# Kernel tuning notes

Hardware: AMD Instinct MI355X
Metric: run time of the kernel (lower is better)

## Reference

```python
import jax, jax.numpy as jnp
import numpy as np

B, T, I = 256, 64, 512
H, C = 512, 97
MAXLEN = 25


def setup_inputs() -> dict:
    key = jax.random.key(0)
    ks = jax.random.split(key, 10)
    s_i = 1.0 / np.sqrt(I)
    s_h = 1.0 / np.sqrt(H)
    s_x = 1.0 / np.sqrt(I + C)
    return {
        "batch_hidden": jax.random.normal(ks[0], (B, T, I), jnp.float32),
        "context": jax.random.randint(ks[1], (B, MAXLEN + 1), 0, C),
        "max_length": MAXLEN,
        "train_mode": 1,
        "W_i2h": jax.random.normal(ks[2], (H, I), jnp.float32) * s_i,
        "W_h2h": jax.random.normal(ks[3], (H, H), jnp.float32) * s_h,
        "b_h2h": jnp.zeros((H,), jnp.float32),
        "w_score": jax.random.normal(ks[4], (1, H), jnp.float32) * s_h,
        "W_ih": jax.random.normal(ks[5], (4 * H, I + C), jnp.float32) * s_x,
        "b_ih": jnp.zeros((4 * H,), jnp.float32),
        "W_hh": jax.random.normal(ks[6], (4 * H, H), jnp.float32) * s_h,
        "b_hh": jnp.zeros((4 * H,), jnp.float32),
        "W_cls": jax.random.normal(ks[7], (C, H), jnp.float32) * s_h,
        "b_cls": jnp.zeros((C,), jnp.float32),
    }


def reference(batch_hidden, context, max_length, train_mode,
              W_i2h, W_h2h, b_h2h, w_score,
              W_ih, b_ih, W_hh, b_hh, W_cls, b_cls):
    steps = int(max_length) + 1
    b, t, _ = batch_hidden.shape
    h_dim = W_h2h.shape[0]
    n_cls = W_cls.shape[0]
    dt = batch_hidden.dtype

    # input_to_hidden(batch_hidden) is step-independent: hoist out of the loop.
    proj = jnp.einsum('bti,hi->bth', batch_hidden, W_i2h)  # [B,T,H]
    sv = w_score[0]  # [H]

    def cell(h, c, onehot):
        prev_proj = h @ W_h2h.T + b_h2h                       # [B,H]
        score = jnp.einsum('bth,h->bt', jnp.tanh(proj + prev_proj[:, None, :]), sv)
        attn = jax.nn.softmax(score, axis=1)                  # [B,T]
        ctx = jnp.einsum('bt,bti->bi', attn, batch_hidden)    # [B,I]
        x = jnp.concatenate([ctx, onehot], axis=1)            # [B,I+C]
        gates = x @ W_ih.T + b_ih + h @ W_hh.T + b_hh          # [B,4H]
        i_g, f_g, g_g, o_g = jnp.split(gates, 4, axis=1)
        c_new = jax.nn.sigmoid(f_g) * c + jax.nn.sigmoid(i_g) * jnp.tanh(g_g)
        h_new = jax.nn.sigmoid(o_g) * jnp.tanh(c_new)
        return h_new, c_new

    h0 = jnp.zeros((b, h_dim), dt)
    c0 = jnp.zeros((b, h_dim), dt)

    if train_mode:
        onehots = jax.nn.one_hot(context.T[:steps], n_cls, dtype=dt)  # [steps,B,C]

        def step(carry, oh):
            h, c = carry
            h, c = cell(h, c, oh)
            return (h, c), h

        _, hs = jax.lax.scan(step, (h0, c0), onehots)
        hidden_outputs = jnp.transpose(hs, (1, 0, 2))          # [B,steps,H]
        probs = hidden_outputs @ W_cls.T + b_cls               # [B,steps,C]
    else:
        def step(carry, _):
            h, c, tgt = carry
            oh = jax.nn.one_hot(tgt, n_cls, dtype=dt)
            h, c = cell(h, c, oh)
            p = h @ W_cls.T + b_cls
            return (h, c, jnp.argmax(p, axis=1)), p

        tgt0 = jnp.zeros((b,), jnp.int32)
        _, ps = jax.lax.scan(step, (h0, c0, tgt0), None, length=steps)
        probs = jnp.transpose(ps, (1, 0, 2))
    return probs
```

## Files before the change

kernel.cpp:

```cpp
#include <hip/hip_runtime.h>

#define BB 256
#define TT 64
#define HH 512
#define CC 97
#define SS 26
#define KX 1024

typedef __attribute__((ext_vector_type(8))) short short8;
typedef __attribute__((ext_vector_type(4))) float f32x4;

#define MFMA16(a, b, c) __builtin_amdgcn_mfma_f32_16x16x32_bf16((a), (b), (c), 0, 0, 0)

__device__ __forceinline__ unsigned short f2bf(float x) {
  unsigned int u = __float_as_uint(x);
  u += 0x7FFFu + ((u >> 16) & 1u);
  return (unsigned short)(u >> 16);
}
__device__ __forceinline__ float bf2f(unsigned short b) {
  return __uint_as_float(((unsigned int)b) << 16);
}
__device__ __forceinline__ void split8(float4 a, float4 b, short8& vh, short8& vl) {
  float x[8] = {a.x, a.y, a.z, a.w, b.x, b.y, b.z, b.w};
#pragma unroll
  for (int i = 0; i < 8; ++i) {
    unsigned short h = f2bf(x[i]);
    vh[i] = (short)h;
    vl[i] = (short)f2bf(x[i] - bf2f(h));
  }
}

__global__ __launch_bounds__(256) void k_init(float4* __restrict__ p, int n4) {
  int i = blockIdx.x * 256 + threadIdx.x;
  if (i < n4) p[i] = make_float4(0.f, 0.f, 0.f, 0.f);
}

__global__ __launch_bounds__(256) void k_prep_wp(const float* __restrict__ W_ih, const float* __restrict__ b_ih,
                                                 const float* __restrict__ W_hh, const float* __restrict__ b_hh,
                                                 unsigned short* __restrict__ Wp_hi, unsigned short* __restrict__ Wp_lo,
                                                 float* __restrict__ bp2, float* __restrict__ Woh2) {
  int p = blockIdx.x;
  int ntile = p >> 6, q = (p >> 4) & 3, jl = p & 15;
  int g = q * 512 + ntile * 16 + jl;
  int tid = threadIdx.x;
  for (int k = tid; k < 1024; k += 256) {
    float v = (k < 512) ? W_ih[(size_t)g * 609 + k] : W_hh[(size_t)g * 512 + (k - 512)];
    unsigned short h = f2bf(v);
    Wp_hi[(size_t)p * 1024 + k] = h;
    Wp_lo[(size_t)p * 1024 + k] = f2bf(v - bf2f(h));
  }
  if (tid < CC) Woh2[(size_t)p * CC + tid] = W_ih[(size_t)g * 609 + 512 + tid];
  if (tid == 0) bp2[p] = b_ih[g] + b_hh[g];
}

__global__ __launch_bounds__(256) void k_prep_w2h(const float* __restrict__ W_h2h,
                                                  unsigned short* __restrict__ Whi, unsigned short* __restrict__ Wlo) {
  int n = blockIdx.x;
  int tid = threadIdx.x;
  for (int k = tid; k < 512; k += 256) {
    float v = W_h2h[(size_t)n * 512 + k];
    unsigned short h = f2bf(v);
    Whi[(size_t)n * 512 + k] = h;
    Wlo[(size_t)n * 512 + k] = f2bf(v - bf2f(h));
  }
}

__global__ __launch_bounds__(256) void k0_proj(const float* __restrict__ A, const float* __restrict__ Bw,
                                               unsigned short* __restrict__ projb) {
  __shared__ short Ah[128][40], Al[128][40], Bh[64][40], Bl[64][40];
  int mt = blockIdx.x >> 3, nt = blockIdx.x & 7;
  int m0 = mt * 128, n0 = nt * 64;
  int tid = threadIdx.x;
  int w = tid >> 6, l = tid & 63;
  int wm = w >> 1, wn = w & 1;
  f32x4 acc[4][2];
#pragma unroll
  for (int i = 0; i < 4; ++i)
#pragma unroll
    for (int j = 0; j < 2; ++j) acc[i][j] = (f32x4){0.f, 0.f, 0.f, 0.f};
  int ar_s = tid >> 1, akc = (tid & 1) * 16;
  int br_s = tid >> 2, bkc = (tid & 3) * 8;
  for (int k0 = 0; k0 < 512; k0 += 32) {
    {
      const float* s = &A[(size_t)(m0 + ar_s) * 512 + k0 + akc];
      short8 vh, vl;
      split8(*(const float4*)s, *(const float4*)(s + 4), vh, vl);
      *(short8*)&Ah[ar_s][akc] = vh; *(short8*)&Al[ar_s][akc] = vl;
      split8(*(const float4*)(s + 8), *(const float4*)(s + 12), vh, vl);
      *(short8*)&Ah[ar_s][akc + 8] = vh; *(short8*)&Al[ar_s][akc + 8] = vl;
      const float* sb = &Bw[(size_t)(n0 + br_s) * 512 + k0 + bkc];
      split8(*(const float4*)sb, *(const float4*)(sb + 4), vh, vl);
      *(short8*)&Bh[br_s][bkc] = vh; *(short8*)&Bl[br_s][bkc] = vl;
    }
    __syncthreads();
    int ko = (l >> 4) * 8;
    short8 ah[4], al8[4];
#pragma unroll
    for (int mf = 0; mf < 4; ++mf) {
      int ar = wm * 64 + mf * 16 + (l & 15);
      ah[mf] = *(short8*)&Ah[ar][ko];
      al8[mf] = *(short8*)&Al[ar][ko];
    }
#pragma unroll
    for (int nf = 0; nf < 2; ++nf) {
      int br = wn * 32 + nf * 16 + (l & 15);
      short8 bh8 = *(short8*)&Bh[br][ko];
      short8 bl8 = *(short8*)&Bl[br][ko];
#pragma unroll
      for (int mf = 0; mf < 4; ++mf) {
        acc[mf][nf] = MFMA16(ah[mf], bh8, acc[mf][nf]);
        acc[mf][nf] = MFMA16(ah[mf], bl8, acc[mf][nf]);
        acc[mf][nf] = MFMA16(al8[mf], bh8, acc[mf][nf]);
      }
    }
    __syncthreads();
  }
#pragma unroll
  for (int mf = 0; mf < 4; ++mf)
#pragma unroll
    for (int nf = 0; nf < 2; ++nf)
#pragma unroll
      for (int r = 0; r < 4; ++r) {
        int m = m0 + wm * 64 + mf * 16 + (l >> 4) * 4 + r;
        int n = n0 + wn * 32 + nf * 16 + (l & 15);
        projb[(size_t)m * 512 + n] = f2bf(acc[mf][nf][r]);
      }
}

__global__ __launch_bounds__(256) void k1_pp(const float* __restrict__ xc, const unsigned short* __restrict__ Whi,
                                             const unsigned short* __restrict__ Wlo, float* __restrict__ pp) {
  __shared__ short Ah[64][40], Al[64][40], Bh[64][40], Bl[64][40];
  int bt = blockIdx.x & 3, nt = blockIdx.x >> 2;
  int b0 = bt * 64, n0 = nt * 64;
  int tid = threadIdx.x, w = tid >> 6, l = tid & 63;
  int wm = w >> 1, wn = w & 1;
  f32x4 acc[2][2];
#pragma unroll
  for (int i = 0; i < 2; ++i)
#pragma unroll
    for (int j = 0; j < 2; ++j) acc[i][j] = (f32x4){0.f, 0.f, 0.f, 0.f};
  int row = tid >> 2, kc = (tid & 3) * 8;
  for (int k0 = 0; k0 < 512; k0 += 32) {
    {
      const float* s = &xc[(size_t)(b0 + row) * KX + 512 + k0 + kc];
      short8 vh, vl;
      split8(*(const float4*)s, *(const float4*)(s + 4), vh, vl);
      *(short8*)&Ah[row][kc] = vh; *(short8*)&Al[row][kc] = vl;
      *(short8*)&Bh[row][kc] = *(const short8*)&Whi[(size_t)(n0 + row) * 512 + k0 + kc];
      *(short8*)&Bl[row][kc] = *(const short8*)&Wlo[(size_t)(n0 + row) * 512 + k0 + kc];
    }
    __syncthreads();
    int ko = (l >> 4) * 8;
    short8 ah[2], al8[2];
#pragma unroll
    for (int mf = 0; mf < 2; ++mf) {
      int ar = wm * 32 + mf * 16 + (l & 15);
      ah[mf] = *(short8*)&Ah[ar][ko];
      al8[mf] = *(short8*)&Al[ar][ko];
    }
#pragma unroll
    for (int nf = 0; nf < 2; ++nf) {
      int br = wn * 32 + nf * 16 + (l & 15);
      short8 bh8 = *(short8*)&Bh[br][ko];
      short8 bl8 = *(short8*)&Bl[br][ko];
#pragma unroll
      for (int mf = 0; mf < 2; ++mf) {
        acc[mf][nf] = MFMA16(ah[mf], bh8, acc[mf][nf]);
        acc[mf][nf] = MFMA16(ah[mf], bl8, acc[mf][nf]);
        acc[mf][nf] = MFMA16(al8[mf], bh8, acc[mf][nf]);
      }
    }
    __syncthreads();
  }
#pragma unroll
  for (int mf = 0; mf < 2; ++mf)
#pragma unroll
    for (int nf = 0; nf < 2; ++nf)
#pragma unroll
      for (int r = 0; r < 4; ++r) {
        int m = b0 + wm * 32 + mf * 16 + (l >> 4) * 4 + r;
        int n = n0 + wn * 32 + nf * 16 + (l & 15);
        pp[(size_t)m * 512 + n] = acc[mf][nf][r];
      }
}

__global__ __launch_bounds__(256) void k2_attn(const unsigned short* __restrict__ projb, const float* __restrict__ pp,
                                               const float* __restrict__ b_h2h, const float* __restrict__ w_score,
                                               const float* __restrict__ bh, float* __restrict__ xc) {
  int b = blockIdx.x;
  __shared__ float sc_s[64];
  int tid = threadIdx.x;
  int wave = tid >> 6, lane = tid & 63;
  float ppv[8], svv[8];
  {
    const float* p0 = &pp[(size_t)b * 512 + lane * 8];
    float4 a0 = *(const float4*)p0, a1 = *(const float4*)(p0 + 4);
    float4 c0 = *(const float4*)&b_h2h[lane * 8], c1 = *(const float4*)&b_h2h[lane * 8 + 4];
    float4 d0 = *(const float4*)&w_score[lane * 8], d1 = *(const float4*)&w_score[lane * 8 + 4];
    ppv[0] = a0.x + c0.x; ppv[1] = a0.y + c0.y; ppv[2] = a0.z + c0.z; ppv[3] = a0.w + c0.w;
    ppv[4] = a1.x + c1.x; ppv[5] = a1.y + c1.y; ppv[6] = a1.z + c1.z; ppv[7] = a1.w + c1.w;
    svv[0] = d0.x; svv[1] = d0.y; svv[2] = d0.z; svv[3] = d0.w;
    svv[4] = d1.x; svv[5] = d1.y; svv[6] = d1.z; svv[7] = d1.w;
  }
  for (int t = wave; t < 64; t += 4) {
    const unsigned short* pr = &projb[((size_t)b * 64 + t) * 512 + lane * 8];
    uint4 raw = *(const uint4*)pr;
    unsigned int uu[4] = {raw.x, raw.y, raw.z, raw.w};
    float acc = 0.f;
#pragma unroll
    for (int i = 0; i < 4; ++i) {
      float f0 = bf2f((unsigned short)(uu[i] & 0xFFFFu));
      float f1 = bf2f((unsigned short)(uu[i] >> 16));
      acc += tanhf(f0 + ppv[2 * i]) * svv[2 * i];
      acc += tanhf(f1 + ppv[2 * i + 1]) * svv[2 * i + 1];
    }
#pragma unroll
    for (int off = 32; off > 0; off >>= 1) acc += __shfl_down(acc, off);
    if (lane == 0) sc_s[t] = acc;
  }
  __syncthreads();
  if (wave == 0) {
    float x = sc_s[lane];
    float m = x;
#pragma unroll
    for (int off = 32; off > 0; off >>= 1) m = fmaxf(m, __shfl_xor(m, off));
    float e = __expf(x - m);
    float ssum = e;
#pragma unroll
    for (int off = 32; off > 0; off >>= 1) ssum += __shfl_xor(ssum, off);
    sc_s[lane] = e / ssum;
  }
  __syncthreads();
  float a0 = 0.f, a1 = 0.f;
  for (int t = 0; t < 64; ++t) {
    float wgt = sc_s[t];
    const float* pb = &bh[((size_t)b * 64 + t) * 512];
    a0 += wgt * pb[tid];
    a1 += wgt * pb[tid + 256];
  }
  xc[(size_t)b * KX + tid] = a0;
  xc[(size_t)b * KX + tid + 256] = a1;
}

__global__ __launch_bounds__(256) void k3_gates(const float* __restrict__ xc, float* __restrict__ xn,
                                                const unsigned short* __restrict__ Wp_hi, const unsigned short* __restrict__ Wp_lo,
                                                const float* __restrict__ bp2, const float* __restrict__ Woh2,
                                                const int* __restrict__ ctxids, float* __restrict__ cbuf,
                                                float* __restrict__ hs, int s) {
  __shared__ short Ah[64][40], Al[64][40], Bh[64][40], Bl[64][40];
  __shared__ int cid_s[64];
  int bt = blockIdx.x & 3, ntile = blockIdx.x >> 2;
  int b0 = bt * 64, n0 = ntile * 64, jb = ntile * 16;
  int tid = threadIdx.x, w = tid >> 6, l = tid & 63;
  if (tid < 64) cid_s[tid] = ctxids[(size_t)(b0 + tid) * SS + s];
  f32x4 acc[4];
#pragma unroll
  for (int i = 0; i < 4; ++i) acc[i] = (f32x4){0.f, 0.f, 0.f, 0.f};
  int row = tid >> 2, kc = (tid & 3) * 8;
  for (int k0 = 0; k0 < 1024; k0 += 32) {
    {
      const float* sp = &xc[(size_t)(b0 + row) * KX + k0 + kc];
      short8 vh, vl;
      split8(*(const float4*)sp, *(const float4*)(sp + 4), vh, vl);
      *(short8*)&Ah[row][kc] = vh; *(short8*)&Al[row][kc] = vl;
      *(short8*)&Bh[row][kc] = *(const short8*)&Wp_hi[(size_t)(n0 + row) * 1024 + k0 + kc];
      *(short8*)&Bl[row][kc] = *(const short8*)&Wp_lo[(size_t)(n0 + row) * 1024 + k0 + kc];
    }
    __syncthreads();
    int ko = (l >> 4) * 8;
    int ar = w * 16 + (l & 15);
    short8 ah = *(short8*)&Ah[ar][ko];
    short8 al8 = *(short8*)&Al[ar][ko];
#pragma unroll
    for (int nf = 0; nf < 4; ++nf) {
      int br = nf * 16 + (l & 15);
      short8 bh8 = *(short8*)&Bh[br][ko];
      short8 bl8 = *(short8*)&Bl[br][ko];
      acc[nf] = MFMA16(ah, bh8, acc[nf]);
      acc[nf] = MFMA16(ah, bl8, acc[nf]);
      acc[nf] = MFMA16(al8, bh8, acc[nf]);
    }
    __syncthreads();
  }
  int jl = l & 15, j = jb + jl;
  float bia[4];
#pragma unroll
  for (int q = 0; q < 4; ++q) bia[q] = bp2[n0 + q * 16 + jl];
#pragma unroll
  for (int r = 0; r < 4; ++r) {
    int br_ = b0 + w * 16 + (l >> 4) * 4 + r;
    int cid = cid_s[w * 16 + (l >> 4) * 4 + r];
    float gi = acc[0][r] + bia[0] + Woh2[(size_t)(n0 + 0 + jl) * CC + cid];
    float gf = acc[1][r] + bia[1] + Woh2[(size_t)(n0 + 16 + jl) * CC + cid];
    float gg = acc[2][r] + bia[2] + Woh2[(size_t)(n0 + 32 + jl) * CC + cid];
    float go = acc[3][r] + bia[3] + Woh2[(size_t)(n0 + 48 + jl) * CC + cid];
    float iv = 1.f / (1.f + __expf(-gi));
    float fv = 1.f / (1.f + __expf(-gf));
    float gv = tanhf(gg);
    float ov = 1.f / (1.f + __expf(-go));
    float cNew = fv * cbuf[(size_t)br_ * HH + j] + iv * gv;
    cbuf[(size_t)br_ * HH + j] = cNew;
    float hv = ov * tanhf(cNew);
    xn[(size_t)br_ * KX + 512 + j] = hv;
    hs[((size_t)br_ * SS + s) * HH + j] = hv;
  }
}

__global__ __launch_bounds__(256) void k4_cls(const float* __restrict__ hsb, const float* __restrict__ Wc,
                                              const float* __restrict__ bc, float* __restrict__ out) {
  __shared__ float Hs[32][36];
  __shared__ float Wcs[112][36];
  int bs0 = blockIdx.x * 32;
  int tid = threadIdx.x;
  int rt = tid >> 4, ct = tid & 15;
  float acc[2][7] = {};
  for (int k0 = 0; k0 < 512; k0 += 32) {
    {
      int row = tid >> 3, kc = (tid & 7) * 4;
      float4 v = *(const float4*)&hsb[(size_t)(bs0 + row) * 512 + k0 + kc];
      Hs[row][kc] = v.x; Hs[row][kc + 1] = v.y; Hs[row][kc + 2] = v.z; Hs[row][kc + 3] = v.w;
    }
    for (int i = tid; i < 776; i += 256) {
      int n = i >> 3, kc = (i & 7) * 4;
      float4 v = *(const float4*)&Wc[(size_t)n * 512 + k0 + kc];
      Wcs[n][kc] = v.x; Wcs[n][kc + 1] = v.y; Wcs[n][kc + 2] = v.z; Wcs[n][kc + 3] = v.w;
    }
    __syncthreads();
#pragma unroll 4
    for (int kk = 0; kk < 32; ++kk) {
      float a0 = Hs[2 * rt][kk], a1 = Hs[2 * rt + 1][kk];
#pragma unroll
      for (int cc = 0; cc < 7; ++cc) {
        float wv = Wcs[ct * 7 + cc][kk];
        acc[0][cc] += a0 * wv;
        acc[1][cc] += a1 * wv;
      }
    }
    __syncthreads();
  }
#pragma unroll
  for (int rr = 0; rr < 2; ++rr)
#pragma unroll
    for (int cc = 0; cc < 7; ++cc) {
      int c = ct * 7 + cc;
      if (c < CC) out[(size_t)(bs0 + 2 * rt + rr) * CC + c] = acc[rr][cc] + bc[c];
    }
}

extern "C" void kernel_launch(void* const* d_in, const int* in_sizes, int n_in,
                              void* d_out, int out_size, void* d_ws, size_t ws_size,
                              hipStream_t stream) {
  const float* bh      = (const float*)d_in[0];
  const int*   ctxi    = (const int*)d_in[1];
  const float* W_i2h   = (const float*)d_in[4];
  const float* W_h2h   = (const float*)d_in[5];
  const float* b_h2h   = (const float*)d_in[6];
  const float* w_score = (const float*)d_in[7];
  const float* W_ih    = (const float*)d_in[8];
  const float* b_ih    = (const float*)d_in[9];
  const float* W_hh    = (const float*)d_in[10];
  const float* b_hh    = (const float*)d_in[11];
  const float* W_cls   = (const float*)d_in[12];
  const float* b_cls   = (const float*)d_in[13];
  float* out = (float*)d_out;

  float* xA   = (float*)d_ws;
  float* xB   = xA + (size_t)BB * KX;
  float* cbuf = xB + (size_t)BB * KX;
  float* pp   = cbuf + (size_t)BB * HH;
  float* hsb  = pp + (size_t)BB * HH;
  unsigned short* projb  = (unsigned short*)(hsb + (size_t)BB * SS * HH);
  unsigned short* Wp_hi  = projb + (size_t)16384 * 512;
  unsigned short* Wp_lo  = Wp_hi + (size_t)2048 * 1024;
  unsigned short* W2h_hi = Wp_lo + (size_t)2048 * 1024;
  unsigned short* W2h_lo = W2h_hi + (size_t)512 * 512;
  float* bp2  = (float*)(W2h_lo + (size_t)512 * 512);
  float* Woh2 = bp2 + 2048;

  k_init<<<dim3(640), dim3(256), 0, stream>>>((float4*)d_ws, 163840);
  k_prep_wp<<<dim3(2048), dim3(256), 0, stream>>>(W_ih, b_ih, W_hh, b_hh, Wp_hi, Wp_lo, bp2, Woh2);
  k_prep_w2h<<<dim3(512), dim3(256), 0, stream>>>(W_h2h, W2h_hi, W2h_lo);
  k0_proj<<<dim3(1024), dim3(256), 0, stream>>>(bh, W_i2h, projb);

  for (int s = 0; s < SS; ++s) {
    float* xc = (s & 1) ? xB : xA;
    float* xn = (s & 1) ? xA : xB;
    k1_pp<<<dim3(32), dim3(256), 0, stream>>>(xc, W2h_hi, W2h_lo, pp);
    k2_attn<<<dim3(256), dim3(256), 0, stream>>>(projb, pp, b_h2h, w_score, bh, xc);
    k3_gates<<<dim3(128), dim3(256), 0, stream>>>(xc, xn, Wp_hi, Wp_lo, bp2, Woh2, ctxi, cbuf, hsb, s);
  }
  k4_cls<<<dim3(208), dim3(256), 0, stream>>>(hsb, W_cls, b_cls, out);
}
```

Measured before the change: 2.271 ms.

## Fuse per-step recurrent kernels into one persistent kernel with grid barriers

Replaces the 78 per-step launches of the pp, attention and gate kernels with a single persistent 256-block kernel. It loops over all steps and uses an atomic-counter grid barrier between phases, which removes launch overhead and inter-kernel gaps. The classifier is also rewritten to use split-bf16 MFMA with pre-split weights, placed in the pp buffer after the loop. The spin barrier relies on all 256 blocks being co-resident, and it serializes phases in which most blocks sit idle.

After: 3.192 ms. 1.41x slower.

```diff
diff --git a/kernel.cpp b/kernel.cpp
--- a/kernel.cpp
+++ b/kernel.cpp
@@ -6,6 +6,7 @@
 #define CC 97
 #define SS 26
 #define KX 1024
+#define GRIDN 256
 
 typedef __attribute__((ext_vector_type(8))) short short8;
 typedef __attribute__((ext_vector_type(4))) float f32x4;
@@ -28,6 +29,18 @@
     vh[i] = (short)h;
     vl[i] = (short)f2bf(x[i] - bf2f(h));
   }
+}
+
+__device__ __forceinline__ void gbar(unsigned* bar) {
+  __syncthreads();
+  if (threadIdx.x == 0) {
+    __threadfence();
+    unsigned t = atomicAdd(bar, 1u);
+    unsigned target = (t / GRIDN + 1u) * GRIDN;
+    while (atomicAdd(bar, 0u) < target) __builtin_amdgcn_s_sleep(2);
+    __threadfence();
+  }
+  __syncthreads();
 }
 
 __global__ __launch_bounds__(256) void k_init(float4* __restrict__ p, int n4) {
@@ -62,6 +75,18 @@
     unsigned short h = f2bf(v);
     Whi[(size_t)n * 512 + k] = h;
     Wlo[(size_t)n * 512 + k] = f2bf(v - bf2f(h));
+  }
+}
+
+__global__ __launch_bounds__(256) void k_prep_wc(const float* __restrict__ Wc,
+                                                 unsigned short* __restrict__ Wc_hi, unsigned short* __restrict__ Wc_lo) {
+  int n = blockIdx.x;
+  int tid = threadIdx.x;
+  for (int k = tid; k < 512; k += 256) {
+    float v = (n < CC) ? Wc[(size_t)n * 512 + k] : 0.f;
+    unsigned short h = f2bf(v);
+    Wc_hi[(size_t)n * 512 + k] = h;
+    Wc_lo[(size_t)n * 512 + k] = f2bf(v - bf2f(h));
   }
 }
 
@@ -127,223 +152,240 @@
       }
 }
 
-__global__ __launch_bounds__(256) void k1_pp(const float* __restrict__ xc, const unsigned short* __restrict__ Whi,
-                                             const unsigned short* __restrict__ Wlo, float* __restrict__ pp) {
+__global__ __launch_bounds__(256) void k_loop(
+    const unsigned short* __restrict__ projb,
+    const unsigned short* __restrict__ W2h_hi, const unsigned short* __restrict__ W2h_lo,
+    const unsigned short* __restrict__ Wp_hi, const unsigned short* __restrict__ Wp_lo,
+    const float* __restrict__ bp2, const float* __restrict__ Woh2,
+    const float* __restrict__ b_h2h, const float* __restrict__ w_score,
+    const float* __restrict__ bh, const int* __restrict__ ctxids,
+    float* __restrict__ xA, float* __restrict__ xB, float* __restrict__ cbuf,
+    float* __restrict__ pp, float* __restrict__ hsb, unsigned* __restrict__ bar) {
   __shared__ short Ah[64][40], Al[64][40], Bh[64][40], Bl[64][40];
-  int bt = blockIdx.x & 3, nt = blockIdx.x >> 2;
-  int b0 = bt * 64, n0 = nt * 64;
+  __shared__ float sc_s[64];
+  __shared__ int cid_s[64];
+  int bid = blockIdx.x, tid = threadIdx.x;
+  int w = tid >> 6, l = tid & 63;
+
+  for (int s = 0; s < SS; ++s) {
+    float* xc = (s & 1) ? xB : xA;
+    float* xn = (s & 1) ? xA : xB;
+
+    if (bid < 32) {
+      int bt = bid & 3, nt = bid >> 2;
+      int b0 = bt * 64, n0 = nt * 64;
+      int wm = w >> 1, wn = w & 1;
+      f32x4 acc[2][2];
+#pragma unroll
+      for (int i = 0; i < 2; ++i)
+#pragma unroll
+        for (int j = 0; j < 2; ++j) acc[i][j] = (f32x4){0.f, 0.f, 0.f, 0.f};
+      int row = tid >> 2, kc = (tid & 3) * 8;
+      for (int k0 = 0; k0 < 512; k0 += 32) {
+        {
+          const float* sp = &xc[(size_t)(b0 + row) * KX + 512 + k0 + kc];
+          short8 vh, vl;
+          split8(*(const float4*)sp, *(const float4*)(sp + 4), vh, vl);
+          *(short8*)&Ah[row][kc] = vh; *(short8*)&Al[row][kc] = vl;
+          *(short8*)&Bh[row][kc] = *(const short8*)&W2h_hi[(size_t)(n0 + row) * 512 + k0 + kc];
+          *(short8*)&Bl[row][kc] = *(const short8*)&W2h_lo[(size_t)(n0 + row) * 512 + k0 + kc];
+        }
+        __syncthreads();
+        int ko = (l >> 4) * 8;
+        short8 ah[2], al8[2];
+#pragma unroll
+        for (int mf = 0; mf < 2; ++mf) {
+          int ar = wm * 32 + mf * 16 + (l & 15);
+          ah[mf] = *(short8*)&Ah[ar][ko];
+          al8[mf] = *(short8*)&Al[ar][ko];
+        }
+#pragma unroll
+        for (int nf = 0; nf < 2; ++nf) {
+          int br = wn * 32 + nf * 16 + (l & 15);
+          short8 bh8 = *(short8*)&Bh[br][ko];
+          short8 bl8 = *(short8*)&Bl[br][ko];
+#pragma unroll
+          for (int mf = 0; mf < 2; ++mf) {
+            acc[mf][nf] = MFMA16(ah[mf], bh8, acc[mf][nf]);
+            acc[mf][nf] = MFMA16(ah[mf], bl8, acc[mf][nf]);
+            acc[mf][nf] = MFMA16(al8[mf], bh8, acc[mf][nf]);
+          }
+        }
+        __syncthreads();
+      }
+#pragma unroll
+      for (int mf = 0; mf < 2; ++mf)
+#pragma unroll
+        for (int nf = 0; nf < 2; ++nf)
+#pragma unroll
+          for (int r = 0; r < 4; ++r) {
+            int m = b0 + wm * 32 + mf * 16 + (l >> 4) * 4 + r;
+            int n = n0 + wn * 32 + nf * 16 + (l & 15);
+            pp[(size_t)m * HH + n] = acc[mf][nf][r];
+          }
+    }
+    gbar(bar);
+
+    {
+      int b = bid;
+      float ppv[8], svv[8];
+      {
+        int l8 = l * 8;
+        const float* p0 = &pp[(size_t)b * HH + l8];
+        float4 a0 = *(const float4*)p0, a1 = *(const float4*)(p0 + 4);
+        float4 c0 = *(const float4*)&b_h2h[l8], c1 = *(const float4*)&b_h2h[l8 + 4];
+        float4 d0 = *(const float4*)&w_score[l8], d1 = *(const float4*)&w_score[l8 + 4];
+        ppv[0] = a0.x + c0.x; ppv[1] = a0.y + c0.y; ppv[2] = a0.z + c0.z; ppv[3] = a0.w + c0.w;
+        ppv[4] = a1.x + c1.x; ppv[5] = a1.y + c1.y; ppv[6] = a1.z + c1.z; ppv[7] = a1.w + c1.w;
+        svv[0] = d0.x; svv[1] = d0.y; svv[2] = d0.z; svv[3] = d0.w;
+        svv[4] = d1.x; svv[5] = d1.y; svv[6] = d1.z; svv[7] = d1.w;
+      }
+      for (int t = w; t < 64; t += 4) {
+        const unsigned short* pr = &projb[((size_t)b * 64 + t) * 512 + l * 8];
+        uint4 raw = *(const uint4*)pr;
+        unsigned int uu[4] = {raw.x, raw.y, raw.z, raw.w};
+        float acc = 0.f;
+#pragma unroll
+        for (int i = 0; i < 4; ++i) {
+          float f0 = bf2f((unsigned short)(uu[i] & 0xFFFFu));
+          float f1 = bf2f((unsigned short)(uu[i] >> 16));
+          acc += tanhf(f0 + ppv[2 * i]) * svv[2 * i];
+          acc += tanhf(f1 + ppv[2 * i + 1]) * svv[2 * i + 1];
+        }
+#pragma unroll
+        for (int off = 32; off > 0; off >>= 1) acc += __shfl_down(acc, off);
+        if (l == 0) sc_s[t] = acc;
+      }
+      __syncthreads();
+      if (w == 0) {
+        float x = sc_s[l];
+        float m = x;
+#pragma unroll
+        for (int off = 32; off > 0; off >>= 1) m = fmaxf(m, __shfl_xor(m, off));
+        float e = __expf(x - m);
+        float ssum = e;
+#pragma unroll
+        for (int off = 32; off > 0; off >>= 1) ssum += __shfl_xor(ssum, off);
+        sc_s[l] = e / ssum;
+      }
+      __syncthreads();
+      float a0 = 0.f, a1 = 0.f;
+      for (int t = 0; t < 64; ++t) {
+        float wgt = sc_s[t];
+        const float* pb = &bh[((size_t)b * 64 + t) * 512];
+        a0 += wgt * pb[tid];
+        a1 += wgt * pb[tid + 256];
+      }
+      xc[(size_t)b * KX + tid] = a0;
+      xc[(size_t)b * KX + tid + 256] = a1;
+    }
+    gbar(bar);
+
+    if (bid < 128) {
+      int bt = bid & 3, ntile = bid >> 2;
+      int b0 = bt * 64, n0 = ntile * 64, jb = ntile * 16;
+      if (tid < 64) cid_s[tid] = ctxids[(size_t)(b0 + tid) * SS + s];
+      f32x4 acc[4];
+#pragma unroll
+      for (int i = 0; i < 4; ++i) acc[i] = (f32x4){0.f, 0.f, 0.f, 0.f};
+      int row = tid >> 2, kc = (tid & 3) * 8;
+      for (int k0 = 0; k0 < 1024; k0 += 32) {
+        {
+          const float* sp = &xc[(size_t)(b0 + row) * KX + k0 + kc];
+          short8 vh, vl;
+          split8(*(const float4*)sp, *(const float4*)(sp + 4), vh, vl);
+          *(short8*)&Ah[row][kc] = vh; *(short8*)&Al[row][kc] = vl;
+          *(short8*)&Bh[row][kc] = *(const short8*)&Wp_hi[(size_t)(n0 + row) * 1024 + k0 + kc];
+          *(short8*)&Bl[row][kc] = *(const short8*)&Wp_lo[(size_t)(n0 + row) * 1024 + k0 + kc];
+        }
+        __syncthreads();
+        int ko = (l >> 4) * 8;
+        int ar = w * 16 + (l & 15);
+        short8 ah = *(short8*)&Ah[ar][ko];
+        short8 al8 = *(short8*)&Al[ar][ko];
+#pragma unroll
+        for (int nf = 0; nf < 4; ++nf) {
+          int br = nf * 16 + (l & 15);
+          short8 bh8 = *(short8*)&Bh[br][ko];
+          short8 bl8 = *(short8*)&Bl[br][ko];
+          acc[nf] = MFMA16(ah, bh8, acc[nf]);
+          acc[nf] = MFMA16(ah, bl8, acc[nf]);
+          acc[nf] = MFMA16(al8, bh8, acc[nf]);
+        }
+        __syncthreads();
+      }
+      int jl = l & 15, j = jb + jl;
+      float bia[4];
+#pragma unroll
+      for (int q = 0; q < 4; ++q) bia[q] = bp2[n0 + q * 16 + jl];
+#pragma unroll
+      for (int r = 0; r < 4; ++r) {
+        int br_ = b0 + w * 16 + (l >> 4) * 4 + r;
+        int cid = cid_s[w * 16 + (l >> 4) * 4 + r];
+        float gi = acc[0][r] + bia[0] + Woh2[(size_t)(n0 + 0 + jl) * CC + cid];
+        float gf = acc[1][r] + bia[1] + Woh2[(size_t)(n0 + 16 + jl) * CC + cid];
+        float gg = acc[2][r] + bia[2] + Woh2[(size_t)(n0 + 32 + jl) * CC + cid];
+        float go = acc[3][r] + bia[3] + Woh2[(size_t)(n0 + 48 + jl) * CC + cid];
+        float iv = 1.f / (1.f + __expf(-gi));
+        float fv = 1.f / (1.f + __expf(-gf));
+        float gv = tanhf(gg);
+        float ov = 1.f / (1.f + __expf(-go));
+        float cNew = fv * cbuf[(size_t)br_ * HH + j] + iv * gv;
+        cbuf[(size_t)br_ * HH + j] = cNew;
+        float hv = ov * tanhf(cNew);
+        xn[(size_t)br_ * KX + 512 + j] = hv;
+        hsb[((size_t)br_ * SS + s) * HH + j] = hv;
+      }
+    }
+    gbar(bar);
+  }
+}
+
+__global__ __launch_bounds__(256) void k4_cls(const float* __restrict__ hsb,
+                                              const unsigned short* __restrict__ Wc_hi,
+                                              const unsigned short* __restrict__ Wc_lo,
+                                              const float* __restrict__ bc, float* __restrict__ out) {
+  __shared__ short Ah[64][40], Al[64][40];
+  __shared__ short Bh[112][40], Bl[112][40];
+  int m0 = blockIdx.x * 64;
   int tid = threadIdx.x, w = tid >> 6, l = tid & 63;
-  int wm = w >> 1, wn = w & 1;
-  f32x4 acc[2][2];
-#pragma unroll
-  for (int i = 0; i < 2; ++i)
-#pragma unroll
-    for (int j = 0; j < 2; ++j) acc[i][j] = (f32x4){0.f, 0.f, 0.f, 0.f};
+  f32x4 acc[7];
+#pragma unroll
+  for (int i = 0; i < 7; ++i) acc[i] = (f32x4){0.f, 0.f, 0.f, 0.f};
   int row = tid >> 2, kc = (tid & 3) * 8;
   for (int k0 = 0; k0 < 512; k0 += 32) {
     {
-      const float* s = &xc[(size_t)(b0 + row) * KX + 512 + k0 + kc];
-      short8 vh, vl;
-      split8(*(const float4*)s, *(const float4*)(s + 4), vh, vl);
-      *(short8*)&Ah[row][kc] = vh; *(short8*)&Al[row][kc] = vl;
-      *(short8*)&Bh[row][kc] = *(const short8*)&Whi[(size_t)(n0 + row) * 512 + k0 + kc];
-      *(short8*)&Bl[row][kc] = *(const short8*)&Wlo[(size_t)(n0 + row) * 512 + k0 + kc];
-    }
-    __syncthreads();
-    int ko = (l >> 4) * 8;
-    short8 ah[2], al8[2];
-#pragma unroll
-    for (int mf = 0; mf < 2; ++mf) {
-      int ar = wm * 32 + mf * 16 + (l & 15);
-      ah[mf] = *(short8*)&Ah[ar][ko];
-      al8[mf] = *(short8*)&Al[ar][ko];
-    }
-#pragma unroll
-    for (int nf = 0; nf < 2; ++nf) {
-      int br = wn * 32 + nf * 16 + (l & 15);
-      short8 bh8 = *(short8*)&Bh[br][ko];
-      short8 bl8 = *(short8*)&Bl[br][ko];
-#pragma unroll
-      for (int mf = 0; mf < 2; ++mf) {
-        acc[mf][nf] = MFMA16(ah[mf], bh8, acc[mf][nf]);
-        acc[mf][nf] = MFMA16(ah[mf], bl8, acc[mf][nf]);
-        acc[mf][nf] = MFMA16(al8[mf], bh8, acc[mf][nf]);
-      }
-    }
-    __syncthreads();
-  }
-#pragma unroll
-  for (int mf = 0; mf < 2; ++mf)
-#pragma unroll
-    for (int nf = 0; nf < 2; ++nf)
-#pragma unroll
-      for (int r = 0; r < 4; ++r) {
-        int m = b0 + wm * 32 + mf * 16 + (l >> 4) * 4 + r;
-        int n = n0 + wn * 32 + nf * 16 + (l & 15);
-        pp[(size_t)m * 512 + n] = acc[mf][nf][r];
-      }
-}
-
-__global__ __launch_bounds__(256) void k2_attn(const unsigned short* __restrict__ projb, const float* __restrict__ pp,
-                                               const float* __restrict__ b_h2h, const float* __restrict__ w_score,
-                                               const float* __restrict__ bh, float* __restrict__ xc) {
-  int b = blockIdx.x;
-  __shared__ float sc_s[64];
-  int tid = threadIdx.x;
-  int wave = tid >> 6, lane = tid & 63;
-  float ppv[8], svv[8];
-  {
-    const float* p0 = &pp[(size_t)b * 512 + lane * 8];
-    float4 a0 = *(const float4*)p0, a1 = *(const float4*)(p0 + 4);
-    float4 c0 = *(const float4*)&b_h2h[lane * 8], c1 = *(const float4*)&b_h2h[lane * 8 + 4];
-    float4 d0 = *(const float4*)&w_score[lane * 8], d1 = *(const float4*)&w_score[lane * 8 + 4];
-    ppv[0] = a0.x + c0.x; ppv[1] = a0.y + c0.y; ppv[2] = a0.z + c0.z; ppv[3] = a0.w + c0.w;
-    ppv[4] = a1.x + c1.x; ppv[5] = a1.y + c1.y; ppv[6] = a1.z + c1.z; ppv[7] = a1.w + c1.w;
-    svv[0] = d0.x; svv[1] = d0.y; svv[2] = d0.z; svv[3] = d0.w;
-    svv[4] = d1.x; svv[5] = d1.y; svv[6] = d1.z; svv[7] = d1.w;
-  }
-  for (int t = wave; t < 64; t += 4) {
-    const unsigned short* pr = &projb[((size_t)b * 64 + t) * 512 + lane * 8];
-    uint4 raw = *(const uint4*)pr;
-    unsigned int uu[4] = {raw.x, raw.y, raw.z, raw.w};
-    float acc = 0.f;
-#pragma unroll
-    for (int i = 0; i < 4; ++i) {
-      float f0 = bf2f((unsigned short)(uu[i] & 0xFFFFu));
-      float f1 = bf2f((unsigned short)(uu[i] >> 16));
-      acc += tanhf(f0 + ppv[2 * i]) * svv[2 * i];
-      acc += tanhf(f1 + ppv[2 * i + 1]) * svv[2 * i + 1];
-    }
-#pragma unroll
-    for (int off = 32; off > 0; off >>= 1) acc += __shfl_down(acc, off);
-    if (lane == 0) sc_s[t] = acc;
-  }
-  __syncthreads();
-  if (wave == 0) {
-    float x = sc_s[lane];
-    float m = x;
-#pragma unroll
-    for (int off = 32; off > 0; off >>= 1) m = fmaxf(m, __shfl_xor(m, off));
-    float e = __expf(x - m);
-    float ssum = e;
-#pragma unroll
-    for (int off = 32; off > 0; off >>= 1) ssum += __shfl_xor(ssum, off);
-    sc_s[lane] = e / ssum;
-  }
-  __syncthreads();
-  float a0 = 0.f, a1 = 0.f;
-  for (int t = 0; t < 64; ++t) {
-    float wgt = sc_s[t];
-    const float* pb = &bh[((size_t)b * 64 + t) * 512];
-    a0 += wgt * pb[tid];
-    a1 += wgt * pb[tid + 256];
-  }
-  xc[(size_t)b * KX + tid] = a0;
-  xc[(size_t)b * KX + tid + 256] = a1;
-}
-
-__global__ __launch_bounds__(256) void k3_gates(const float* __restrict__ xc, float* __restrict__ xn,
-                                                const unsigned short* __restrict__ Wp_hi, const unsigned short* __restrict__ Wp_lo,
-                                                const float* __restrict__ bp2, const float* __restrict__ Woh2,
-                                                const int* __restrict__ ctxids, float* __restrict__ cbuf,
-                                                float* __restrict__ hs, int s) {
-  __shared__ short Ah[64][40], Al[64][40], Bh[64][40], Bl[64][40];
-  __shared__ int cid_s[64];
-  int bt = blockIdx.x & 3, ntile = blockIdx.x >> 2;
-  int b0 = bt * 64, n0 = ntile * 64, jb = ntile * 16;
-  int tid = threadIdx.x, w = tid >> 6, l = tid & 63;
-  if (tid < 64) cid_s[tid] = ctxids[(size_t)(b0 + tid) * SS + s];
-  f32x4 acc[4];
-#pragma unroll
-  for (int i = 0; i < 4; ++i) acc[i] = (f32x4){0.f, 0.f, 0.f, 0.f};
-  int row = tid >> 2, kc = (tid & 3) * 8;
-  for (int k0 = 0; k0 < 1024; k0 += 32) {
-    {
-      const float* sp = &xc[(size_t)(b0 + row) * KX + k0 + kc];
+      const float* sp = &hsb[(size_t)(m0 + row) * 512 + k0 + kc];
       short8 vh, vl;
       split8(*(const float4*)sp, *(const float4*)(sp + 4), vh, vl);
       *(short8*)&Ah[row][kc] = vh; *(short8*)&Al[row][kc] = vl;
-      *(short8*)&Bh[row][kc] = *(const short8*)&Wp_hi[(size_t)(n0 + row) * 1024 + k0 + kc];
-      *(short8*)&Bl[row][kc] = *(const short8*)&Wp_lo[(size_t)(n0 + row) * 1024 + k0 + kc];
+    }
+    for (int i = tid; i < 448; i += 256) {
+      int r = i >> 2, kb = (i & 3) * 8;
+      *(short8*)&Bh[r][kb] = *(const short8*)&Wc_hi[(size_t)r * 512 + k0 + kb];
+      *(short8*)&Bl[r][kb] = *(const short8*)&Wc_lo[(size_t)r * 512 + k0 + kb];
     }
     __syncthreads();
     int ko = (l >> 4) * 8;
-    int ar = w * 16 + (l & 15);
-    short8 ah = *(short8*)&Ah[ar][ko];
-    short8 al8 = *(short8*)&Al[ar][ko];
-#pragma unroll
-    for (int nf = 0; nf < 4; ++nf) {
-      int br = nf * 16 + (l & 15);
-      short8 bh8 = *(short8*)&Bh[br][ko];
-      short8 bl8 = *(short8*)&Bl[br][ko];
+    short8 ah = *(short8*)&Ah[w * 16 + (l & 15)][ko];
+    short8 al8 = *(short8*)&Al[w * 16 + (l & 15)][ko];
+#pragma unroll
+    for (int nf = 0; nf < 7; ++nf) {
+      short8 bh8 = *(short8*)&Bh[nf * 16 + (l & 15)][ko];
+      short8 bl8 = *(short8*)&Bl[nf * 16 + (l & 15)][ko];
       acc[nf] = MFMA16(ah, bh8, acc[nf]);
       acc[nf] = MFMA16(ah, bl8, acc[nf]);
       acc[nf] = MFMA16(al8, bh8, acc[nf]);
     }
     __syncthreads();
   }
-  int jl = l & 15, j = jb + jl;
-  float bia[4];
-#pragma unroll
-  for (int q = 0; q < 4; ++q) bia[q] = bp2[n0 + q * 16 + jl];
-#pragma unroll
-  for (int r = 0; r < 4; ++r) {
-    int br_ = b0 + w * 16 + (l >> 4) * 4 + r;
-    int cid = cid_s[w * 16 + (l >> 4) * 4 + r];
-    float gi = acc[0][r] + bia[0] + Woh2[(size_t)(n0 + 0 + jl) * CC + cid];
-    float gf = acc[1][r] + bia[1] + Woh2[(size_t)(n0 + 16 + jl) * CC + cid];
-    float gg = acc[2][r] + bia[2] + Woh2[(size_t)(n0 + 32 + jl) * CC + cid];
-    float go = acc[3][r] + bia[3] + Woh2[(size_t)(n0 + 48 + jl) * CC + cid];
-    float iv = 1.f / (1.f + __expf(-gi));
-    float fv = 1.f / (1.f + __expf(-gf));
-    float gv = tanhf(gg);
-    float ov = 1.f / (1.f + __expf(-go));
-    float cNew = fv * cbuf[(size_t)br_ * HH + j] + iv * gv;
-    cbuf[(size_t)br_ * HH + j] = cNew;
-    float hv = ov * tanhf(cNew);
-    xn[(size_t)br_ * KX + 512 + j] = hv;
-    hs[((size_t)br_ * SS + s) * HH + j] = hv;
-  }
-}
-
-__global__ __launch_bounds__(256) void k4_cls(const float* __restrict__ hsb, const float* __restrict__ Wc,
-                                              const float* __restrict__ bc, float* __restrict__ out) {
-  __shared__ float Hs[32][36];
-  __shared__ float Wcs[112][36];
-  int bs0 = blockIdx.x * 32;
-  int tid = threadIdx.x;
-  int rt = tid >> 4, ct = tid & 15;
-  float acc[2][7] = {};
-  for (int k0 = 0; k0 < 512; k0 += 32) {
-    {
-      int row = tid >> 3, kc = (tid & 7) * 4;
-      float4 v = *(const float4*)&hsb[(size_t)(bs0 + row) * 512 + k0 + kc];
-      Hs[row][kc] = v.x; Hs[row][kc + 1] = v.y; Hs[row][kc + 2] = v.z; Hs[row][kc + 3] = v.w;
-    }
-    for (int i = tid; i < 776; i += 256) {
-      int n = i >> 3, kc = (i & 7) * 4;
-      float4 v = *(const float4*)&Wc[(size_t)n * 512 + k0 + kc];
-      Wcs[n][kc] = v.x; Wcs[n][kc + 1] = v.y; Wcs[n][kc + 2] = v.z; Wcs[n][kc + 3] = v.w;
-    }
-    __syncthreads();
-#pragma unroll 4
-    for (int kk = 0; kk < 32; ++kk) {
-      float a0 = Hs[2 * rt][kk], a1 = Hs[2 * rt + 1][kk];
-#pragma unroll
-      for (int cc = 0; cc < 7; ++cc) {
-        float wv = Wcs[ct * 7 + cc][kk];
-        acc[0][cc] += a0 * wv;
-        acc[1][cc] += a1 * wv;
-      }
-    }
-    __syncthreads();
-  }
-#pragma unroll
-  for (int rr = 0; rr < 2; ++rr)
-#pragma unroll
-    for (int cc = 0; cc < 7; ++cc) {
-      int c = ct * 7 + cc;
-      if (c < CC) out[(size_t)(bs0 + 2 * rt + rr) * CC + c] = acc[rr][cc] + bc[c];
+#pragma unroll
+  for (int nf = 0; nf < 7; ++nf)
+#pragma unroll
+    for (int r = 0; r < 4; ++r) {
+      int m = m0 + w * 16 + (l >> 4) * 4 + r;
+      int n = nf * 16 + (l & 15);
+      if (n < CC) out[(size_t)m * CC + n] = acc[nf][r] + bc[n];
     }
 }
 
@@ -367,7 +409,8 @@
   float* xA   = (float*)d_ws;
   float* xB   = xA + (size_t)BB * KX;
   float* cbuf = xB + (size_t)BB * KX;
-  float* pp   = cbuf + (size_t)BB * HH;
+  unsigned* bar = (unsigned*)(cbuf + (size_t)BB * HH);
+  float* pp   = (float*)bar + 64;
   float* hsb  = pp + (size_t)BB * HH;
   unsigned short* projb  = (unsigned short*)(hsb + (size_t)BB * SS * HH);
   unsigned short* Wp_hi  = projb + (size_t)16384 * 512;
@@ -376,18 +419,18 @@
   unsigned short* W2h_lo = W2h_hi + (size_t)512 * 512;
   float* bp2  = (float*)(W2h_lo + (size_t)512 * 512);
   float* Woh2 = bp2 + 2048;
-
-  k_init<<<dim3(640), dim3(256), 0, stream>>>((float4*)d_ws, 163840);
+  unsigned short* Wc_hi = (unsigned short*)pp;
+  unsigned short* Wc_lo = Wc_hi + (size_t)112 * 512;
+
+  k_init<<<dim3(641), dim3(256), 0, stream>>>((float4*)d_ws, 163856);
   k_prep_wp<<<dim3(2048), dim3(256), 0, stream>>>(W_ih, b_ih, W_hh, b_hh, Wp_hi, Wp_lo, bp2, Woh2);
   k_prep_w2h<<<dim3(512), dim3(256), 0, stream>>>(W_h2h, W2h_hi, W2h_lo);
   k0_proj<<<dim3(1024), dim3(256), 0, stream>>>(bh, W_i2h, projb);
 
-  for (int s = 0; s < SS; ++s) {
-    float* xc = (s & 1) ? xB : xA;
-    float* xn = (s & 1) ? xA : xB;
-    k1_pp<<<dim3(32), dim3(256), 0, stream>>>(xc, W2h_hi, W2h_lo, pp);
-    k2_attn<<<dim3(256), dim3(256), 0, stream>>>(projb, pp, b_h2h, w_score, bh, xc);
-    k3_gates<<<dim3(128), dim3(256), 0, stream>>>(xc, xn, Wp_hi, Wp_lo, bp2, Woh2, ctxi, cbuf, hsb, s);
-  }
-  k4_cls<<<dim3(208), dim3(256), 0, stream>>>(hsb, W_cls, b_cls, out);
-}
+  k_loop<<<dim3(GRIDN), dim3(256), 0, stream>>>(
+      projb, W2h_hi, W2h_lo, Wp_hi, Wp_lo, bp2, Woh2,
+      b_h2h, w_score, bh, ctxi, xA, xB, cbuf, pp, hsb, bar);
+
+  k_prep_wc<<<dim3(112), dim3(256), 0, stream>>>(W_cls, Wc_hi, Wc_lo);
+  k4_cls<<<dim3(104), dim3(256), 0, stream>>>(hsb, Wc_hi, Wc_lo, b_cls, out);
+}
```
